# Kernel optimization log

Measured on AMD Instinct MI355X. Metric: run time of the kernel, lower is better.

Reference implementation:

```python
import jax, jax.numpy as jnp
import numpy as np

jax.config.update("jax_enable_x64", True)  # original casts to double for Sinkhorn

SINKHORN_EPS = 0.003
SINKHORN_ITER = 50
MU = 0.25


def setup_inputs() -> dict:
    key = jax.random.key(0)
    k1, k2 = jax.random.split(key)
    x = jax.random.normal(k1, (4096, 4096), dtype=jnp.float32)        # [B, D]
    codebook = jax.random.normal(k2, (256, 4096), dtype=jnp.float32)  # [K, D]
    return {"x": x, "codebook": codebook}


def _sinkhorn_probs(d2term):
    # d2term: [B, K] squared distances (float32)
    B, K = d2term.shape
    max_d = jnp.max(d2term, axis=-1, keepdims=True)
    min_d = jnp.min(d2term, axis=-1, keepdims=True)
    mid_d = (max_d + min_d) / 2
    normed = ((d2term - mid_d) / (max_d - mid_d + 1e-8)).astype(jnp.float64)
    standard = jnp.exp(-normed / SINKHORN_EPS)
    standard = standard / standard.sum()  # sum over dim1 then dim0 == total sum

    def body(i, carry):
        s, n = carry
        s = s / s.sum(axis=0, keepdims=True)
        n = n / K
        s = s / s.sum(axis=1, keepdims=True)
        n = n / B
        return (s, n)

    standard, normed = jax.lax.fori_loop(0, SINKHORN_ITER, body, (standard, normed))
    # original returns d2term_normed * B as probs (d2term_standard is unused after loop)
    return normed * B


def reference(x, codebook):
    # squared euclidean distances: [B, K]
    d2term = (jnp.sum(x * x, axis=-1, keepdims=True)
              + jnp.sum(codebook * codebook, axis=-1)[None, :]
              - 2.0 * (x @ codebook.T))
    probs = _sinkhorn_probs(d2term)              # [B, K] float64
    indices = jnp.argmax(probs, axis=-1)         # [B] int
    quant_hard = codebook[indices]               # [B, D] gather
    # straight-through estimator
    quant = jax.lax.stop_gradient(quant_hard - x) + x
    codebook_loss = jnp.mean((quant_hard - jax.lax.stop_gradient(x)) ** 2, axis=-1)
    commitment_loss = jnp.mean((jax.lax.stop_gradient(quant_hard) - x) ** 2, axis=-1)
    loss = codebook_loss + MU * commitment_loss  # [B]
    return quant, indices, probs, loss
```

## Files before the change

### kernel.cpp

```cpp
#include <hip/hip_runtime.h>
#include <hip/hip_bf16.h>
#include <math.h>

#define D_DIM   4096
#define B_ROWS  4096
#define K_CODES 256
#define MARGIN  3.0
#define KS      4
#define KSLICE  (D_DIM / KS)
#define BK      64
#define NITER   (KSLICE / BK)

#define IDX_OFF   (B_ROWS * D_DIM)
#define PROBS_OFF (IDX_OFF + B_ROWS)
#define LOSS_OFF  (PROBS_OFF + B_ROWS * K_CODES)

typedef __bf16 bf16x8 __attribute__((ext_vector_type(8)));
typedef float  f32x16 __attribute__((ext_vector_type(16)));

#define PART_ELEMS ((size_t)KS * B_ROWS * K_CODES)

static __device__ inline unsigned short f2bf(float f) {
    __hip_bfloat16 h = __float2bfloat16(f);
    return *reinterpret_cast<unsigned short*>(&h);
}

__global__ __launch_bounds__(256) void prep_cb(const float* __restrict__ cb,
                                               unsigned short* __restrict__ cbsw,
                                               double* __restrict__ cc) {
    const int lane = threadIdx.x & 63;
    const int k = blockIdx.x * 4 + (threadIdx.x >> 6);
    const float4* row4 = (const float4*)(cb + (size_t)k * D_DIM);
    double a0 = 0.0, a1 = 0.0, a2 = 0.0, a3 = 0.0;
#pragma unroll
    for (int i = 0; i < 16; ++i) {
        float4 v = row4[i * 64 + lane];
        a0 += (double)v.x * v.x; a1 += (double)v.y * v.y;
        a2 += (double)v.z * v.z; a3 += (double)v.w * v.w;
        ushort4 h;
        h.x = f2bf(v.x); h.y = f2bf(v.y); h.z = f2bf(v.z); h.w = f2bf(v.w);
        const int c = (i * 64 + lane) * 4;
        const int panel = c >> 6, q = (c >> 3) & 7, off = c & 7;
        *(ushort4*)&cbsw[(((size_t)panel * 8 + q) * K_CODES + k) * 8 + off] = h;
    }
    double s = (a0 + a1) + (a2 + a3);
    for (int off = 32; off; off >>= 1) s += __shfl_xor(s, off);
    if (lane == 0) cc[k] = s;
}

__global__ __launch_bounds__(256, 4) void gemm(const float* __restrict__ x,
                                               const unsigned short* __restrict__ cbsw,
                                               float* __restrict__ part,
                                               float* __restrict__ xxp) {
    __shared__ unsigned short As[8 * 32 * 8];
    __shared__ unsigned short Bs[8 * K_CODES * 8];
    const int t = threadIdx.x;
    const int lane = t & 63, w = t >> 6;
    const int h = lane >> 5, mr = lane & 31;
    const int m0 = blockIdx.x * 32;
    const int ks = blockIdx.y;
    const int k0 = ks * KSLICE;

    const int arow = t >> 3, acg = 4 * (t & 7);
    const float* ag = x + (size_t)(m0 + arow) * D_DIM + k0 + acg;
    unsigned short* aw0 = &As[(((acg >> 3)    ) * 32 + arow) * 8 + (acg & 7)];
    unsigned short* aw1 = &As[(((acg >> 3) + 4) * 32 + arow) * 8 + (acg & 7)];
    const unsigned short* bg = cbsw + (size_t)(ks * NITER) * 16384 + t * 8;

    f32x16 acc0, acc1;
#pragma unroll
    for (int i = 0; i < 16; ++i) { acc0[i] = 0.f; acc1[i] = 0.f; }
    float sq = 0.f;

    float4 a0 = *(const float4*)(ag);
    float4 a1 = *(const float4*)(ag + 32);
    for (int it = 0; it < NITER; ++it) {
        const int kn = (it + 1 < NITER) ? (it + 1) * BK : 0;
        float4 n0 = *(const float4*)(ag + kn);
        float4 n1 = *(const float4*)(ag + kn + 32);
        __syncthreads();
#pragma unroll
        for (int r = 0; r < 8; ++r)
            __builtin_amdgcn_global_load_lds(
                (const __attribute__((address_space(1))) void*)(bg + (size_t)it * 16384 + r * 2048),
                (__attribute__((address_space(3))) void*)(&Bs[(t + 256 * r) * 8]),
                16, 0, 0);
        ushort4 h0, h1;
        h0.x = f2bf(a0.x); h0.y = f2bf(a0.y); h0.z = f2bf(a0.z); h0.w = f2bf(a0.w);
        h1.x = f2bf(a1.x); h1.y = f2bf(a1.y); h1.z = f2bf(a1.z); h1.w = f2bf(a1.w);
        *(ushort4*)aw0 = h0;
        *(ushort4*)aw1 = h1;
        sq += a0.x*a0.x + a0.y*a0.y + a0.z*a0.z + a0.w*a0.w
            + a1.x*a1.x + a1.y*a1.y + a1.z*a1.z + a1.w*a1.w;
        __syncthreads();
#pragma unroll
        for (int s = 0; s < 4; ++s) {
            const int q = 2 * s + h;
            bf16x8 af = *(const bf16x8*)&As[(q * 32 + mr) * 8];
            bf16x8 b0 = *(const bf16x8*)&Bs[(q * K_CODES + w * 64 + mr) * 8];
            bf16x8 b1 = *(const bf16x8*)&Bs[(q * K_CODES + w * 64 + 32 + mr) * 8];
            acc0 = __builtin_amdgcn_mfma_f32_32x32x16_bf16(af, b0, acc0, 0, 0, 0);
            acc1 = __builtin_amdgcn_mfma_f32_32x32x16_bf16(af, b1, acc1, 0, 0, 0);
        }
        a0 = n0; a1 = n1;
    }

    sq += __shfl_xor(sq, 1);
    sq += __shfl_xor(sq, 2);
    sq += __shfl_xor(sq, 4);
    if ((t & 7) == 0) xxp[(size_t)ks * B_ROWS + m0 + arow] = sq;

    float* dst = part + ((size_t)ks * B_ROWS + m0) * K_CODES + w * 64;
#pragma unroll
    for (int r = 0; r < 16; ++r) {
        const int rowit = (r & 3) + 8 * (r >> 2) + 4 * h;
        dst[(size_t)rowit * K_CODES + mr]      = acc0[r];
        dst[(size_t)rowit * K_CODES + 32 + mr] = acc1[r];
    }
}

__global__ __launch_bounds__(256) void finish(const float* __restrict__ x,
                                              const float* __restrict__ cb,
                                              const float* __restrict__ part,
                                              const double* __restrict__ cc,
                                              const float* __restrict__ xxp,
                                              float* __restrict__ out) {
    const int lane = threadIdx.x & 63;
    const int row = blockIdx.x * 4 + (threadIdx.x >> 6);

    double xx = ((double)xxp[row] + (double)xxp[B_ROWS + row])
              + ((double)xxp[2 * B_ROWS + row] + (double)xxp[3 * B_ROWS + row]);
    float4 p[KS];
#pragma unroll
    for (int s = 0; s < KS; ++s)
        p[s] = ((const float4*)(part + ((size_t)s * B_ROWS + row) * K_CODES))[lane];
    double v[4];
    v[0] = xx + cc[4 * lane + 0] - 2.0 * (((double)p[0].x + p[1].x) + ((double)p[2].x + p[3].x));
    v[1] = xx + cc[4 * lane + 1] - 2.0 * (((double)p[0].y + p[1].y) + ((double)p[2].y + p[3].y));
    v[2] = xx + cc[4 * lane + 2] - 2.0 * (((double)p[0].z + p[1].z) + ((double)p[2].z + p[3].z));
    v[3] = xx + cc[4 * lane + 3] - 2.0 * (((double)p[0].w + p[1].w) + ((double)p[2].w + p[3].w));

    double mx = fmax(fmax(v[0], v[1]), fmax(v[2], v[3]));
    for (int off = 32; off; off >>= 1) mx = fmax(mx, __shfl_xor(mx, off));
    const double thr = mx - MARGIN;

    unsigned long long b[4];
#pragma unroll
    for (int j = 0; j < 4; ++j) b[j] = __ballot(v[j] >= thr);
    const int total = __popcll(b[0]) + __popcll(b[1]) + __popcll(b[2]) + __popcll(b[3]);

    int bestk = 0; double best;
    if (total == 1) {
        best = mx;
#pragma unroll
        for (int j = 0; j < 4; ++j)
            if (b[j]) bestk = 4 * (int)__builtin_ctzll(b[j]) + j;
    } else {
        const float4* xrow4 = (const float4*)(x + (size_t)row * D_DIM);
        int flags = 0;
#pragma unroll
        for (int j = 0; j < 4; ++j) if (v[j] >= thr) flags |= 1 << j;
        unsigned long long cand = __ballot(flags != 0);
        best = -1.0e300;
        while (cand) {
            const int lsrc = __builtin_ctzll(cand);
            cand &= cand - 1;
            const int f = __shfl(flags, lsrc);
            for (int j = 0; j < 4; ++j) {
                if (!((f >> j) & 1)) continue;
                const int k = 4 * lsrc + j;
                const float4* crow4 = (const float4*)(cb + (size_t)k * D_DIM);
                double a0 = 0.0, a1 = 0.0, a2 = 0.0, a3 = 0.0;
#pragma unroll
                for (int i = 0; i < 16; ++i) {
                    float4 xa = xrow4[i * 64 + lane];
                    float4 ca = crow4[i * 64 + lane];
                    a0 += (double)xa.x * ca.x; a1 += (double)xa.y * ca.y;
                    a2 += (double)xa.z * ca.z; a3 += (double)xa.w * ca.w;
                }
                double s = (a0 + a1) + (a2 + a3);
                for (int off = 32; off; off >>= 1) s += __shfl_xor(s, off);
                const double d2e = xx + cc[k] - 2.0 * s;
                if (d2e > best) { best = d2e; bestk = k; }
            }
        }
    }

    if (lane == 0) {
        out[IDX_OFF + row]  = (float)bestk;
        out[LOSS_OFF + row] = (float)(1.25 * best / (double)D_DIM);
    }
    float4 z = make_float4(0.f, 0.f, 0.f, 0.f);
    ((float4*)(out + PROBS_OFF + (size_t)row * K_CODES))[lane] = z;
    const float4* src = (const float4*)(cb + (size_t)bestk * D_DIM);
    float4* dst = (float4*)(out + (size_t)row * D_DIM);
#pragma unroll
    for (int i = 0; i < 16; ++i) dst[i * 64 + lane] = src[i * 64 + lane];
}

extern "C" void kernel_launch(void* const* d_in, const int* in_sizes, int n_in,
                              void* d_out, int out_size, void* d_ws, size_t ws_size,
                              hipStream_t stream) {
    const float* x  = (const float*)d_in[0];
    const float* cb = (const float*)d_in[1];
    float* out = (float*)d_out;

    float*          part = (float*)d_ws;
    unsigned short* cbsw = (unsigned short*)((char*)d_ws + PART_ELEMS * sizeof(float));
    double*         cc   = (double*)((char*)cbsw + (size_t)K_CODES * D_DIM * sizeof(unsigned short));
    float*          xxp  = (float*)(cc + K_CODES);

    hipLaunchKernelGGL(prep_cb, dim3(64),      dim3(256), 0, stream, cb, cbsw, cc);
    hipLaunchKernelGGL(gemm,    dim3(128, KS), dim3(256), 0, stream, x, cbsw, part, xxp);
    hipLaunchKernelGGL(finish,  dim3(1024),    dim3(256), 0, stream, x, cb, part, cc, xxp, out);
}
```

Measured before the change: 155.3 us.

## Double-buffer GEMM LDS tiles to overlap codebook loads with MFMA

Converts the distance GEMM's single-buffered A/B LDS tiles into ping-pong buffers, so the next K-slice of codebook (via global_load_lds) and bf16-converted x rows are written while MFMAs consume the current buffer. The two __syncthreads per iteration become one explicit waitcnt plus barrier, and x is prefetched two iterations ahead. This doubles LDS use and lowers the occupancy hint from 4 to 2 blocks per CU. The hand-written vmcnt(2) wait relies on ordering assumptions about outstanding loads.

```diff
diff --git a/kernel.cpp b/kernel.cpp
--- a/kernel.cpp
+++ b/kernel.cpp
@@ -48,12 +48,12 @@
     if (lane == 0) cc[k] = s;
 }
 
-__global__ __launch_bounds__(256, 4) void gemm(const float* __restrict__ x,
+__global__ __launch_bounds__(256, 2) void gemm(const float* __restrict__ x,
                                                const unsigned short* __restrict__ cbsw,
                                                float* __restrict__ part,
                                                float* __restrict__ xxp) {
-    __shared__ unsigned short As[8 * 32 * 8];
-    __shared__ unsigned short Bs[8 * K_CODES * 8];
+    __shared__ unsigned short As[2][8 * 32 * 8];
+    __shared__ unsigned short Bs[2][8 * K_CODES * 8];
     const int t = threadIdx.x;
     const int lane = t & 63, w = t >> 6;
     const int h = lane >> 5, mr = lane & 31;
@@ -63,8 +63,8 @@
 
     const int arow = t >> 3, acg = 4 * (t & 7);
     const float* ag = x + (size_t)(m0 + arow) * D_DIM + k0 + acg;
-    unsigned short* aw0 = &As[(((acg >> 3)    ) * 32 + arow) * 8 + (acg & 7)];
-    unsigned short* aw1 = &As[(((acg >> 3) + 4) * 32 + arow) * 8 + (acg & 7)];
+    const int aw0 = (((acg >> 3)    ) * 32 + arow) * 8 + (acg & 7);
+    const int aw1 = (((acg >> 3) + 4) * 32 + arow) * 8 + (acg & 7);
     const unsigned short* bg = cbsw + (size_t)(ks * NITER) * 16384 + t * 8;
 
     f32x16 acc0, acc1;
@@ -72,37 +72,67 @@
     for (int i = 0; i < 16; ++i) { acc0[i] = 0.f; acc1[i] = 0.f; }
     float sq = 0.f;
 
-    float4 a0 = *(const float4*)(ag);
-    float4 a1 = *(const float4*)(ag + 32);
+#pragma unroll
+    for (int r = 0; r < 8; ++r)
+        __builtin_amdgcn_global_load_lds(
+            (const __attribute__((address_space(1))) void*)(bg + r * 2048),
+            (__attribute__((address_space(3))) void*)(&Bs[0][(t + 256 * r) * 8]),
+            16, 0, 0);
+    float4 p0 = *(const float4*)(ag);
+    float4 p1 = *(const float4*)(ag + 32);
+    float4 n0 = *(const float4*)(ag + BK);
+    float4 n1 = *(const float4*)(ag + BK + 32);
+    {
+        ushort4 h0, h1;
+        h0.x = f2bf(p0.x); h0.y = f2bf(p0.y); h0.z = f2bf(p0.z); h0.w = f2bf(p0.w);
+        h1.x = f2bf(p1.x); h1.y = f2bf(p1.y); h1.z = f2bf(p1.z); h1.w = f2bf(p1.w);
+        *(ushort4*)&As[0][aw0] = h0;
+        *(ushort4*)&As[0][aw1] = h1;
+        sq += p0.x*p0.x + p0.y*p0.y + p0.z*p0.z + p0.w*p0.w
+            + p1.x*p1.x + p1.y*p1.y + p1.z*p1.z + p1.w*p1.w;
+    }
+    asm volatile("s_waitcnt vmcnt(2) lgkmcnt(0)" ::: "memory");
+    __builtin_amdgcn_s_barrier();
+    __builtin_amdgcn_sched_barrier(0);
+
+#pragma unroll
     for (int it = 0; it < NITER; ++it) {
-        const int kn = (it + 1 < NITER) ? (it + 1) * BK : 0;
-        float4 n0 = *(const float4*)(ag + kn);
-        float4 n1 = *(const float4*)(ag + kn + 32);
-        __syncthreads();
-#pragma unroll
-        for (int r = 0; r < 8; ++r)
-            __builtin_amdgcn_global_load_lds(
-                (const __attribute__((address_space(1))) void*)(bg + (size_t)it * 16384 + r * 2048),
-                (__attribute__((address_space(3))) void*)(&Bs[(t + 256 * r) * 8]),
-                16, 0, 0);
-        ushort4 h0, h1;
-        h0.x = f2bf(a0.x); h0.y = f2bf(a0.y); h0.z = f2bf(a0.z); h0.w = f2bf(a0.w);
-        h1.x = f2bf(a1.x); h1.y = f2bf(a1.y); h1.z = f2bf(a1.z); h1.w = f2bf(a1.w);
-        *(ushort4*)aw0 = h0;
-        *(ushort4*)aw1 = h1;
-        sq += a0.x*a0.x + a0.y*a0.y + a0.z*a0.z + a0.w*a0.w
-            + a1.x*a1.x + a1.y*a1.y + a1.z*a1.z + a1.w*a1.w;
-        __syncthreads();
+        const int p = it & 1, pn = p ^ 1;
+
+        if (it + 1 < NITER) {
+#pragma unroll
+            for (int r = 0; r < 8; ++r)
+                __builtin_amdgcn_global_load_lds(
+                    (const __attribute__((address_space(1))) void*)(bg + (size_t)(it + 1) * 16384 + r * 2048),
+                    (__attribute__((address_space(3))) void*)(&Bs[pn][(t + 256 * r) * 8]),
+                    16, 0, 0);
+            ushort4 h0, h1;
+            h0.x = f2bf(n0.x); h0.y = f2bf(n0.y); h0.z = f2bf(n0.z); h0.w = f2bf(n0.w);
+            h1.x = f2bf(n1.x); h1.y = f2bf(n1.y); h1.z = f2bf(n1.z); h1.w = f2bf(n1.w);
+            *(ushort4*)&As[pn][aw0] = h0;
+            *(ushort4*)&As[pn][aw1] = h1;
+            sq += n0.x*n0.x + n0.y*n0.y + n0.z*n0.z + n0.w*n0.w
+                + n1.x*n1.x + n1.y*n1.y + n1.z*n1.z + n1.w*n1.w;
+        }
+        const int t2 = (it + 2 < NITER) ? (it + 2) * BK : 0;
+        float4 m0v = *(const float4*)(ag + t2);
+        float4 m1v = *(const float4*)(ag + t2 + 32);
+
 #pragma unroll
         for (int s = 0; s < 4; ++s) {
             const int q = 2 * s + h;
-            bf16x8 af = *(const bf16x8*)&As[(q * 32 + mr) * 8];
-            bf16x8 b0 = *(const bf16x8*)&Bs[(q * K_CODES + w * 64 + mr) * 8];
-            bf16x8 b1 = *(const bf16x8*)&Bs[(q * K_CODES + w * 64 + 32 + mr) * 8];
+            bf16x8 af = *(const bf16x8*)&As[p][(q * 32 + mr) * 8];
+            bf16x8 b0 = *(const bf16x8*)&Bs[p][(q * K_CODES + w * 64 + mr) * 8];
+            bf16x8 b1 = *(const bf16x8*)&Bs[p][(q * K_CODES + w * 64 + 32 + mr) * 8];
             acc0 = __builtin_amdgcn_mfma_f32_32x32x16_bf16(af, b0, acc0, 0, 0, 0);
             acc1 = __builtin_amdgcn_mfma_f32_32x32x16_bf16(af, b1, acc1, 0, 0, 0);
         }
-        a0 = n0; a1 = n1;
+
+        asm volatile("s_waitcnt vmcnt(2) lgkmcnt(0)" ::: "memory");
+        __builtin_amdgcn_s_barrier();
+        __builtin_amdgcn_sched_barrier(0);
+
+        n0 = m0v; n1 = m1v;
     }
 
     sq += __shfl_xor(sq, 1);
```

Result: faster. 151.7 us (-2.4%).
